# Kernel tuning notes

Hardware: AMD Instinct MI355X
Metric: run time of the kernel (lower is better)

## Reference

```python
import jax, jax.numpy as jnp
import numpy as np

NUM_GRAPHS = 1024  # B
HIDDEN = 256       # d
N_NODES = 400000
N_ITERS = 6


def setup_inputs() -> dict:
    key = jax.random.key(0)
    ks = jax.random.split(key, 8)
    d = HIDDEN
    feat = jax.random.normal(ks[0], (N_NODES, d), dtype=jnp.float32)
    segment_ids = jnp.sort(jax.random.randint(ks[1], (N_NODES,), 0, NUM_GRAPHS, dtype=jnp.int32))
    s = 0.05
    W_ih = jax.random.normal(ks[2], (4 * d, 2 * d), dtype=jnp.float32) * s
    W_hh = jax.random.normal(ks[3], (4 * d, d), dtype=jnp.float32) * s
    b_ih = jax.random.normal(ks[4], (4 * d,), dtype=jnp.float32) * s
    b_hh = jax.random.normal(ks[5], (4 * d,), dtype=jnp.float32) * s
    fc_w = jax.random.normal(ks[6], (d, 2 * d), dtype=jnp.float32) * s
    fc_b = jax.random.normal(ks[7], (d,), dtype=jnp.float32) * s
    return {"feat": feat, "segment_ids": segment_ids, "W_ih": W_ih, "W_hh": W_hh,
            "b_ih": b_ih, "b_hh": b_hh, "fc_w": fc_w, "fc_b": fc_b}


def _lstm_cell(x, h, c, W_ih, W_hh, b_ih, b_hh):
    # PyTorch gate order: i, f, g, o
    gates = x @ W_ih.T + h @ W_hh.T + b_ih + b_hh  # [B, 4d]
    i, f, g, o = jnp.split(gates, 4, axis=-1)
    c_new = jax.nn.sigmoid(f) * c + jax.nn.sigmoid(i) * jnp.tanh(g)
    h_new = jax.nn.sigmoid(o) * jnp.tanh(c_new)
    return h_new, c_new


def _set2set(feat, segment_ids, W_ih, W_hh, b_ih, b_hh):
    N, d = feat.shape
    B = NUM_GRAPHS
    h = jnp.zeros((B, d), dtype=feat.dtype)
    c = jnp.zeros((B, d), dtype=feat.dtype)
    q_star = jnp.zeros((B, 2 * d), dtype=feat.dtype)
    for _ in range(N_ITERS):  # small fixed iteration count
        h, c = _lstm_cell(q_star, h, c, W_ih, W_hh, b_ih, b_hh)
        q = h  # [B, d]
        e = jnp.sum(feat * q[segment_ids], axis=-1)  # [N]
        seg_max = jax.ops.segment_max(e, segment_ids, num_segments=B)
        seg_max = jax.lax.stop_gradient(seg_max)
        ex = jnp.exp(e - seg_max[segment_ids])
        denom = jax.ops.segment_sum(ex, segment_ids, num_segments=B)
        alpha = ex / denom[segment_ids]  # segment softmax, [N]
        readout = jax.ops.segment_sum(alpha[:, None] * feat, segment_ids, num_segments=B)  # [B, d]
        q_star = jnp.concatenate([q, readout], axis=-1)  # [B, 2d]
    return q_star


def reference(feat, segment_ids, W_ih, W_hh, b_ih, b_hh, fc_w, fc_b):
    q_star = _set2set(feat, segment_ids, W_ih, W_hh, b_ih, b_hh)  # [B, 2d]
    return q_star @ fc_w.T + fc_b  # [B, d]
```

## Files before the change

### kernel.cpp

```cpp
#include <hip/hip_runtime.h>

#define D   256
#define B   1024
#define K2  512
#define G4  1024

__device__ __forceinline__ float sigm(float x)   { return 1.f / (1.f + __expf(-x)); }
__device__ __forceinline__ float tanh_f(float x) { return 1.f - 2.f / (1.f + __expf(2.f * x)); }

__global__ void prep_weights(const float* __restrict__ W_ih, const float* __restrict__ W_hh,
                             const float* __restrict__ b_ih, const float* __restrict__ b_hh,
                             float* __restrict__ Wc, float* __restrict__ bc) {
    int idx = blockIdx.x * blockDim.x + threadIdx.x;
    if (idx < G4 * K2) {
        int j = idx >> 9;
        int k = idx & 511;
        float w = W_ih[idx];
        if (k < D) w += W_hh[j * D + k];
        Wc[idx] = w;
    }
    if (idx < G4) bc[idx] = b_ih[idx] + b_hh[idx];
}

__global__ void seg_bounds(const int* __restrict__ seg, int* __restrict__ out, int N) {
    int b = blockIdx.x * blockDim.x + threadIdx.x;
    if (b > B) return;
    if (b == B) { out[B] = N; return; }
    int lo = 0, hi = N;
    while (lo < hi) {
        int mid = (lo + hi) >> 1;
        if (seg[mid] < b) lo = mid + 1; else hi = mid;
    }
    out[b] = lo;
}

__global__ __launch_bounds__(256) void gemm_nt(const float* __restrict__ A,
                                               const float* __restrict__ Bm,
                                               const float* __restrict__ bias,
                                               float* __restrict__ Cp,
                                               int M, int N, int K, int ksz) {
    __shared__ float As[16][68];
    __shared__ float Bs[16][68];
    int tid = threadIdx.x;
    int tx = tid & 15, ty = tid >> 4;
    int m0 = blockIdx.y << 6, n0 = blockIdx.x << 6;
    int z = blockIdx.z;
    int klo = z * ksz;
    float* C = Cp + (size_t)z * M * N;
    int lr = tid >> 2;
    int lk = (tid & 3) << 2;
    const float* pa = A  + (size_t)(m0 + lr) * K + klo + lk;
    const float* pb = Bm + (size_t)(n0 + lr) * K + klo + lk;
    float4 a4 = *(const float4*)pa;
    float4 b4 = *(const float4*)pb;
    float acc[4][4] = {};
    for (int k0 = 0; k0 < ksz; k0 += 16) {
        As[lk + 0][lr] = a4.x; As[lk + 1][lr] = a4.y; As[lk + 2][lr] = a4.z; As[lk + 3][lr] = a4.w;
        Bs[lk + 0][lr] = b4.x; Bs[lk + 1][lr] = b4.y; Bs[lk + 2][lr] = b4.z; Bs[lk + 3][lr] = b4.w;
        __syncthreads();
        if (k0 + 16 < ksz) {
            a4 = *(const float4*)(pa + k0 + 16);
            b4 = *(const float4*)(pb + k0 + 16);
        }
#pragma unroll
        for (int kk = 0; kk < 16; ++kk) {
            float a0 = As[kk][ty * 4 + 0], a1 = As[kk][ty * 4 + 1];
            float a2 = As[kk][ty * 4 + 2], a3 = As[kk][ty * 4 + 3];
            float b0 = Bs[kk][tx * 4 + 0], b1 = Bs[kk][tx * 4 + 1];
            float b2 = Bs[kk][tx * 4 + 2], b3 = Bs[kk][tx * 4 + 3];
            acc[0][0] += a0 * b0; acc[0][1] += a0 * b1; acc[0][2] += a0 * b2; acc[0][3] += a0 * b3;
            acc[1][0] += a1 * b0; acc[1][1] += a1 * b1; acc[1][2] += a1 * b2; acc[1][3] += a1 * b3;
            acc[2][0] += a2 * b0; acc[2][1] += a2 * b1; acc[2][2] += a2 * b2; acc[2][3] += a2 * b3;
            acc[3][0] += a3 * b0; acc[3][1] += a3 * b1; acc[3][2] += a3 * b2; acc[3][3] += a3 * b3;
        }
        __syncthreads();
    }
    int n = n0 + tx * 4;
    float bx = 0.f, by = 0.f, bz = 0.f, bw = 0.f;
    if (z == 0 && bias) { bx = bias[n]; by = bias[n + 1]; bz = bias[n + 2]; bw = bias[n + 3]; }
#pragma unroll
    for (int i = 0; i < 4; ++i) {
        int m = m0 + ty * 4 + i;
        float4 o;
        o.x = acc[i][0] + bx; o.y = acc[i][1] + by; o.z = acc[i][2] + bz; o.w = acc[i][3] + bw;
        *(float4*)(C + (size_t)m * N + n) = o;
    }
}

__global__ __launch_bounds__(256) void attn(const float* __restrict__ feat,
                                            const int* __restrict__ segs,
                                            const float* __restrict__ gpart,
                                            const float* __restrict__ bc,
                                            float* __restrict__ cbuf,
                                            float* __restrict__ xcat,
                                            float* __restrict__ pm,
                                            float* __restrict__ pl,
                                            float* __restrict__ pacc,
                                            int it) {
    int blk = blockIdx.x, tid = threadIdx.x;
    int b = blk >> 2, sp = blk & 3;
    int wave = tid >> 6, lane = tid & 63;

    __shared__ float h_sh[D];
    __shared__ float pd[4][16][69];
    __shared__ float esh[2][64];
    __shared__ float wsh[2][64];
    __shared__ float acc_sh[4][D];

    {
        int j = tid;
        float gi, gf, gg, go;
        if (it == 0) {
            gi = bc[j]; gf = bc[D + j]; gg = bc[2 * D + j]; go = bc[3 * D + j];
        } else {
            const float* g0 = gpart + (size_t)b * G4;
            const float* g1 = g0 + (size_t)B * G4;
            gi = g0[j]         + g1[j];
            gf = g0[D + j]     + g1[D + j];
            gg = g0[2 * D + j] + g1[2 * D + j];
            go = g0[3 * D + j] + g1[3 * D + j];
        }
        float cold = (it == 0) ? 0.f : cbuf[(size_t)(it & 1) * B * D + (size_t)b * D + j];
        float cn = sigm(gf) * cold + sigm(gi) * tanh_f(gg);
        float hn = sigm(go) * tanh_f(cn);
        cbuf[(size_t)((it & 1) ^ 1) * B * D + (size_t)b * D + j] = cn;
        xcat[(size_t)b * K2 + j] = hn;
        h_sh[j] = hn;
    }
    __syncthreads();
    float4 q4 = *(const float4*)&h_sh[lane * 4];

    int s0 = segs[b], e0 = segs[b + 1];
    int len = e0 - s0, span = (len + 3) >> 2;
    int s = s0 + sp * span;
    int e = min(s + span, e0);

    float m = -3.0e38f, l = 0.f;
    float4 acc = make_float4(0.f, 0.f, 0.f, 0.f);
    int par = 0;

    for (int base = s; base < e; base += 64, par ^= 1) {
        float4 f[16];
#pragma unroll
        for (int t = 0; t < 16; ++t) {
            int n = base + wave * 16 + t;
            f[t] = (n < e) ? *(const float4*)(feat + (size_t)n * D + lane * 4)
                           : make_float4(0.f, 0.f, 0.f, 0.f);
        }
#pragma unroll
        for (int t = 0; t < 16; ++t)
            pd[wave][t][lane] = f[t].x * q4.x + f[t].y * q4.y + f[t].z * q4.z + f[t].w * q4.w;
        int tt = lane & 15, sg = lane >> 4;
        float r = 0.f;
#pragma unroll
        for (int i = 0; i < 16; ++i) r += pd[wave][tt][sg * 16 + i];
        r += __shfl_xor(r, 16, 64);
        r += __shfl_xor(r, 32, 64);
        if (lane < 16) esh[par][wave * 16 + lane] = r;
        __syncthreads();
        float ev = (base + lane < e) ? esh[par][lane] : -3.0e38f;
        float cm = ev;
#pragma unroll
        for (int off = 32; off > 0; off >>= 1) cm = fmaxf(cm, __shfl_xor(cm, off, 64));
        float mc = fmaxf(m, cm);
        float wl = __expf(ev - mc);
        float ws = wl;
#pragma unroll
        for (int off = 32; off > 0; off >>= 1) ws += __shfl_xor(ws, off, 64);
        float sc = __expf(m - mc);
        l = l * sc + ws;
        m = mc;
        acc.x *= sc; acc.y *= sc; acc.z *= sc; acc.w *= sc;
        wsh[par][lane] = wl;
#pragma unroll
        for (int t = 0; t < 16; ++t) {
            float w = wsh[par][wave * 16 + t];
            acc.x = fmaf(w, f[t].x, acc.x);
            acc.y = fmaf(w, f[t].y, acc.y);
            acc.z = fmaf(w, f[t].z, acc.z);
            acc.w = fmaf(w, f[t].w, acc.w);
        }
    }
    acc_sh[wave][lane * 4 + 0] = acc.x;
    acc_sh[wave][lane * 4 + 1] = acc.y;
    acc_sh[wave][lane * 4 + 2] = acc.z;
    acc_sh[wave][lane * 4 + 3] = acc.w;
    __syncthreads();
    float r4 = acc_sh[0][tid] + acc_sh[1][tid] + acc_sh[2][tid] + acc_sh[3][tid];
    pacc[(size_t)blk * D + tid] = r4;
    if (tid == 0) { pm[blk] = m; pl[blk] = l; }
}

__global__ __launch_bounds__(256) void attn_combine(const float* __restrict__ pm,
                                                    const float* __restrict__ pl,
                                                    const float* __restrict__ pacc,
                                                    float* __restrict__ xcat) {
    int b = blockIdx.x, tid = threadIdx.x;
    float m0 = pm[4 * b], m1 = pm[4 * b + 1], m2 = pm[4 * b + 2], m3 = pm[4 * b + 3];
    float M = fmaxf(fmaxf(m0, m1), fmaxf(m2, m3));
    float w0 = __expf(m0 - M), w1 = __expf(m1 - M), w2 = __expf(m2 - M), w3 = __expf(m3 - M);
    float L = pl[4 * b] * w0 + pl[4 * b + 1] * w1 + pl[4 * b + 2] * w2 + pl[4 * b + 3] * w3;
    float R = pacc[(size_t)(4 * b + 0) * D + tid] * w0
            + pacc[(size_t)(4 * b + 1) * D + tid] * w1
            + pacc[(size_t)(4 * b + 2) * D + tid] * w2
            + pacc[(size_t)(4 * b + 3) * D + tid] * w3;
    xcat[(size_t)b * K2 + D + tid] = (L > 0.f) ? R / L : 0.f;
}

extern "C" void kernel_launch(void* const* d_in, const int* in_sizes, int n_in,
                              void* d_out, int out_size, void* d_ws, size_t ws_size,
                              hipStream_t stream) {
    const float* feat   = (const float*)d_in[0];
    const int*   segids = (const int*)d_in[1];
    const float* W_ih   = (const float*)d_in[2];
    const float* W_hh   = (const float*)d_in[3];
    const float* b_ih   = (const float*)d_in[4];
    const float* b_hh   = (const float*)d_in[5];
    const float* fc_w   = (const float*)d_in[6];
    const float* fc_b   = (const float*)d_in[7];
    float* out = (float*)d_out;
    int N = in_sizes[1];

    float* Wc    = (float*)d_ws;
    float* bc    = Wc + (size_t)G4 * K2;
    float* xcat  = bc + G4;
    float* cbuf  = xcat + (size_t)B * K2;
    float* gpart = cbuf + (size_t)2 * B * D;
    float* pm    = gpart + (size_t)2 * B * G4;
    float* pl    = pm + 4 * B;
    float* pacc  = pl + 4 * B;
    int*   segs  = (int*)(pacc + (size_t)4 * B * D);

    hipLaunchKernelGGL(prep_weights, dim3((G4 * K2 + 255) / 256), dim3(256), 0, stream,
                       W_ih, W_hh, b_ih, b_hh, Wc, bc);
    hipLaunchKernelGGL(seg_bounds, dim3((B + 1 + 255) / 256), dim3(256), 0, stream,
                       segids, segs, N);

    for (int it = 0; it < 6; ++it) {
        if (it > 0)
            hipLaunchKernelGGL(gemm_nt, dim3(G4 / 64, B / 64, 2), dim3(256), 0, stream,
                               xcat, Wc, bc, gpart, B, G4, K2, K2 / 2);
        hipLaunchKernelGGL(attn, dim3(4 * B), dim3(256), 0, stream,
                           feat, segs, gpart, bc, cbuf, xcat, pm, pl, pacc, it);
        hipLaunchKernelGGL(attn_combine, dim3(B), dim3(256), 0, stream, pm, pl, pacc, xcat);
    }
    hipLaunchKernelGGL(gemm_nt, dim3(D / 64, B / 64, 1), dim3(256), 0, stream,
                       xcat, fc_w, fc_b, out, B, D, K2, K2);
}
```

Baseline: 1.109 ms.

## Split LSTM step out of attention, use 8-way node splits and 128x128 GEMM

Moves the LSTM cell update into its own lstm_step kernel so the attention kernel only reads h from xcat. Attention is now split 8 ways per graph instead of 4, and the combine kernel merges 8 partial softmax states. The gate GEMM now uses a 128x128-tile kernel with 8x8 register blocking and a 4-way K split. The aim is more parallelism in the memory-bound attention pass and higher GEMM throughput, at the cost of one extra launch per iteration and more partial buffers to write and reduce.

```diff
diff --git a/kernel.cpp b/kernel.cpp
--- a/kernel.cpp
+++ b/kernel.cpp
@@ -4,6 +4,8 @@
 #define B   1024
 #define K2  512
 #define G4  1024
+#define NSPLIT 8
+#define NZ     4
 
 __device__ __forceinline__ float sigm(float x)   { return 1.f / (1.f + __expf(-x)); }
 __device__ __forceinline__ float tanh_f(float x) { return 1.f - 2.f / (1.f + __expf(2.f * x)); }
@@ -32,6 +34,60 @@
         if (seg[mid] < b) lo = mid + 1; else hi = mid;
     }
     out[b] = lo;
+}
+
+__global__ __launch_bounds__(256) void gemm128(const float* __restrict__ A,
+                                               const float* __restrict__ Bm,
+                                               float* __restrict__ Cp,
+                                               int M, int N, int K, int ksz) {
+    __shared__ float As[16][132];
+    __shared__ float Bs[16][132];
+    int tid = threadIdx.x;
+    int tx = tid & 15, ty = tid >> 4;
+    int m0 = blockIdx.y << 7, n0 = blockIdx.x << 7;
+    int klo = blockIdx.z * ksz;
+    float* C = Cp + (size_t)blockIdx.z * M * N;
+    int lr = tid >> 1;
+    int lk = (tid & 1) << 3;
+    const float* pa = A  + (size_t)(m0 + lr) * K + klo + lk;
+    const float* pb = Bm + (size_t)(n0 + lr) * K + klo + lk;
+    float4 a0 = *(const float4*)pa, a1 = *(const float4*)(pa + 4);
+    float4 b0 = *(const float4*)pb, b1 = *(const float4*)(pb + 4);
+    float acc[8][8] = {};
+    for (int k0 = 0; k0 < ksz; k0 += 16) {
+        As[lk + 0][lr] = a0.x; As[lk + 1][lr] = a0.y; As[lk + 2][lr] = a0.z; As[lk + 3][lr] = a0.w;
+        As[lk + 4][lr] = a1.x; As[lk + 5][lr] = a1.y; As[lk + 6][lr] = a1.z; As[lk + 7][lr] = a1.w;
+        Bs[lk + 0][lr] = b0.x; Bs[lk + 1][lr] = b0.y; Bs[lk + 2][lr] = b0.z; Bs[lk + 3][lr] = b0.w;
+        Bs[lk + 4][lr] = b1.x; Bs[lk + 5][lr] = b1.y; Bs[lk + 6][lr] = b1.z; Bs[lk + 7][lr] = b1.w;
+        __syncthreads();
+        if (k0 + 16 < ksz) {
+            a0 = *(const float4*)(pa + k0 + 16); a1 = *(const float4*)(pa + k0 + 20);
+            b0 = *(const float4*)(pb + k0 + 16); b1 = *(const float4*)(pb + k0 + 20);
+        }
+#pragma unroll
+        for (int kk = 0; kk < 16; ++kk) {
+            float4 alo = *(const float4*)&As[kk][ty * 4];
+            float4 ahi = *(const float4*)&As[kk][ty * 4 + 64];
+            float4 blo = *(const float4*)&Bs[kk][tx * 4];
+            float4 bhi = *(const float4*)&Bs[kk][tx * 4 + 64];
+            float ar[8] = {alo.x, alo.y, alo.z, alo.w, ahi.x, ahi.y, ahi.z, ahi.w};
+            float br[8] = {blo.x, blo.y, blo.z, blo.w, bhi.x, bhi.y, bhi.z, bhi.w};
+#pragma unroll
+            for (int i = 0; i < 8; ++i)
+#pragma unroll
+                for (int j = 0; j < 8; ++j)
+                    acc[i][j] = fmaf(ar[i], br[j], acc[i][j]);
+        }
+        __syncthreads();
+    }
+#pragma unroll
+    for (int i = 0; i < 8; ++i) {
+        int m = m0 + ty * 4 + (i & 3) + ((i >> 2) << 6);
+        float4 o0 = make_float4(acc[i][0], acc[i][1], acc[i][2], acc[i][3]);
+        float4 o1 = make_float4(acc[i][4], acc[i][5], acc[i][6], acc[i][7]);
+        *(float4*)(C + (size_t)m * N + n0 + tx * 4)      = o0;
+        *(float4*)(C + (size_t)m * N + n0 + tx * 4 + 64) = o1;
+    }
 }
 
 __global__ __launch_bounds__(256) void gemm_nt(const float* __restrict__ A,
@@ -87,51 +143,46 @@
     }
 }
 
-__global__ __launch_bounds__(256) void attn(const float* __restrict__ feat,
-                                            const int* __restrict__ segs,
-                                            const float* __restrict__ gpart,
-                                            const float* __restrict__ bc,
-                                            float* __restrict__ cbuf,
-                                            float* __restrict__ xcat,
-                                            float* __restrict__ pm,
-                                            float* __restrict__ pl,
-                                            float* __restrict__ pacc,
-                                            int it) {
+__global__ __launch_bounds__(256) void lstm_step(const float* __restrict__ gpart,
+                                                 const float* __restrict__ bc,
+                                                 float* __restrict__ cbuf,
+                                                 float* __restrict__ xcat,
+                                                 int it) {
+    int b = blockIdx.x, j = threadIdx.x;
+    float gi = bc[j], gf = bc[D + j], gg = bc[2 * D + j], go = bc[3 * D + j];
+    if (it > 0) {
+        const float* g = gpart + (size_t)b * G4;
+#pragma unroll
+        for (int s = 0; s < NZ; ++s, g += (size_t)B * G4) {
+            gi += g[j]; gf += g[D + j]; gg += g[2 * D + j]; go += g[3 * D + j];
+        }
+    }
+    float cold = (it == 0) ? 0.f : cbuf[(size_t)(it & 1) * B * D + (size_t)b * D + j];
+    float cn = sigm(gf) * cold + sigm(gi) * tanh_f(gg);
+    float hn = sigm(go) * tanh_f(cn);
+    cbuf[(size_t)((it & 1) ^ 1) * B * D + (size_t)b * D + j] = cn;
+    xcat[(size_t)b * K2 + j] = hn;
+}
+
+__global__ __launch_bounds__(256) void attn8(const float* __restrict__ feat,
+                                             const int* __restrict__ segs,
+                                             const float* __restrict__ xcat,
+                                             float* __restrict__ pm,
+                                             float* __restrict__ pl,
+                                             float* __restrict__ pacc) {
     int blk = blockIdx.x, tid = threadIdx.x;
-    int b = blk >> 2, sp = blk & 3;
+    int b = blk >> 3, sp = blk & 7;
     int wave = tid >> 6, lane = tid & 63;
 
-    __shared__ float h_sh[D];
     __shared__ float pd[4][16][69];
     __shared__ float esh[2][64];
     __shared__ float wsh[2][64];
     __shared__ float acc_sh[4][D];
 
-    {
-        int j = tid;
-        float gi, gf, gg, go;
-        if (it == 0) {
-            gi = bc[j]; gf = bc[D + j]; gg = bc[2 * D + j]; go = bc[3 * D + j];
-        } else {
-            const float* g0 = gpart + (size_t)b * G4;
-            const float* g1 = g0 + (size_t)B * G4;
-            gi = g0[j]         + g1[j];
-            gf = g0[D + j]     + g1[D + j];
-            gg = g0[2 * D + j] + g1[2 * D + j];
-            go = g0[3 * D + j] + g1[3 * D + j];
-        }
-        float cold = (it == 0) ? 0.f : cbuf[(size_t)(it & 1) * B * D + (size_t)b * D + j];
-        float cn = sigm(gf) * cold + sigm(gi) * tanh_f(gg);
-        float hn = sigm(go) * tanh_f(cn);
-        cbuf[(size_t)((it & 1) ^ 1) * B * D + (size_t)b * D + j] = cn;
-        xcat[(size_t)b * K2 + j] = hn;
-        h_sh[j] = hn;
-    }
-    __syncthreads();
-    float4 q4 = *(const float4*)&h_sh[lane * 4];
+    float4 q4 = *(const float4*)(xcat + (size_t)b * K2 + lane * 4);
 
     int s0 = segs[b], e0 = segs[b + 1];
-    int len = e0 - s0, span = (len + 3) >> 2;
+    int len = e0 - s0, span = (len + NSPLIT - 1) >> 3;
     int s = s0 + sp * span;
     int e = min(s + span, e0);
 
@@ -191,19 +242,21 @@
     if (tid == 0) { pm[blk] = m; pl[blk] = l; }
 }
 
-__global__ __launch_bounds__(256) void attn_combine(const float* __restrict__ pm,
-                                                    const float* __restrict__ pl,
-                                                    const float* __restrict__ pacc,
-                                                    float* __restrict__ xcat) {
+__global__ __launch_bounds__(256) void attn_combine8(const float* __restrict__ pm,
+                                                     const float* __restrict__ pl,
+                                                     const float* __restrict__ pacc,
+                                                     float* __restrict__ xcat) {
     int b = blockIdx.x, tid = threadIdx.x;
-    float m0 = pm[4 * b], m1 = pm[4 * b + 1], m2 = pm[4 * b + 2], m3 = pm[4 * b + 3];
-    float M = fmaxf(fmaxf(m0, m1), fmaxf(m2, m3));
-    float w0 = __expf(m0 - M), w1 = __expf(m1 - M), w2 = __expf(m2 - M), w3 = __expf(m3 - M);
-    float L = pl[4 * b] * w0 + pl[4 * b + 1] * w1 + pl[4 * b + 2] * w2 + pl[4 * b + 3] * w3;
-    float R = pacc[(size_t)(4 * b + 0) * D + tid] * w0
-            + pacc[(size_t)(4 * b + 1) * D + tid] * w1
-            + pacc[(size_t)(4 * b + 2) * D + tid] * w2
-            + pacc[(size_t)(4 * b + 3) * D + tid] * w3;
+    float M = -3.0e38f;
+#pragma unroll
+    for (int s = 0; s < NSPLIT; ++s) M = fmaxf(M, pm[NSPLIT * b + s]);
+    float L = 0.f, R = 0.f;
+#pragma unroll
+    for (int s = 0; s < NSPLIT; ++s) {
+        float w = __expf(pm[NSPLIT * b + s] - M);
+        L += pl[NSPLIT * b + s] * w;
+        R += pacc[(size_t)(NSPLIT * b + s) * D + tid] * w;
+    }
     xcat[(size_t)b * K2 + D + tid] = (L > 0.f) ? R / L : 0.f;
 }
 
@@ -226,10 +279,10 @@
     float* xcat  = bc + G4;
     float* cbuf  = xcat + (size_t)B * K2;
     float* gpart = cbuf + (size_t)2 * B * D;
-    float* pm    = gpart + (size_t)2 * B * G4;
-    float* pl    = pm + 4 * B;
-    float* pacc  = pl + 4 * B;
-    int*   segs  = (int*)(pacc + (size_t)4 * B * D);
+    float* pm    = gpart + (size_t)NZ * B * G4;
+    float* pl    = pm + NSPLIT * B;
+    float* pacc  = pl + NSPLIT * B;
+    int*   segs  = (int*)(pacc + (size_t)NSPLIT * B * D);
 
     hipLaunchKernelGGL(prep_weights, dim3((G4 * K2 + 255) / 256), dim3(256), 0, stream,
                        W_ih, W_hh, b_ih, b_hh, Wc, bc);
@@ -238,11 +291,13 @@
 
     for (int it = 0; it < 6; ++it) {
         if (it > 0)
-            hipLaunchKernelGGL(gemm_nt, dim3(G4 / 64, B / 64, 2), dim3(256), 0, stream,
-                               xcat, Wc, bc, gpart, B, G4, K2, K2 / 2);
-        hipLaunchKernelGGL(attn, dim3(4 * B), dim3(256), 0, stream,
-                           feat, segs, gpart, bc, cbuf, xcat, pm, pl, pacc, it);
-        hipLaunchKernelGGL(attn_combine, dim3(B), dim3(256), 0, stream, pm, pl, pacc, xcat);
+            hipLaunchKernelGGL(gemm128, dim3(G4 / 128, B / 128, NZ), dim3(256), 0, stream,
+                               xcat, Wc, gpart, B, G4, K2, K2 / NZ);
+        hipLaunchKernelGGL(lstm_step, dim3(B), dim3(256), 0, stream,
+                           gpart, bc, cbuf, xcat, it);
+        hipLaunchKernelGGL(attn8, dim3(NSPLIT * B), dim3(256), 0, stream,
+                           feat, segs, xcat, pm, pl, pacc);
+        hipLaunchKernelGGL(attn_combine8, dim3(B), dim3(256), 0, stream, pm, pl, pacc, xcat);
     }
     hipLaunchKernelGGL(gemm_nt, dim3(D / 64, B / 64, 1), dim3(256), 0, stream,
                        xcat, fc_w, fc_b, out, B, D, K2, K2);
```

New measurement: 1.109 ms. About the same (-0.0%).
